# Optimization experiments

Hardware: AMD Instinct MI355X
Metric: run time of the kernel (lower is better)

## Reference

```python
import jax, jax.numpy as jnp
import numpy as np

IN_F = 768
OUT_F = 256
ALPHA = 0.2  # LeakyReLU negative slope
N = 8192


def setup_inputs() -> dict:
    key = jax.random.key(0)
    k_x, k_w, k_a = jax.random.split(key, 3)
    all_token_tensor = jax.random.normal(k_x, (N, IN_F), dtype=jnp.float32)
    # xavier_uniform with gain=1.414 for W [in, out] and a [2*out, 1]
    lim_w = 1.414 * np.sqrt(6.0 / (IN_F + OUT_F))
    W = jax.random.uniform(k_w, (IN_F, OUT_F), minval=-lim_w, maxval=lim_w, dtype=jnp.float32)
    lim_a = 1.414 * np.sqrt(6.0 / (2 * OUT_F + 1))
    a = jax.random.uniform(k_a, (2 * OUT_F, 1), minval=-lim_a, maxval=lim_a, dtype=jnp.float32)
    return {"all_token_tensor": all_token_tensor, "W": W, "a": a}


def reference(all_token_tensor, W, a):
    # Wh: [N, F]
    Wh = all_token_tensor @ W
    # e_ij = leakyrelu([Wh_i ; Wh_j] . a) = leakyrelu(Wh_i.a1 + Wh_j.a2)
    # (identical math to the original's [N,N,2F] concat, without materializing it)
    s1 = Wh @ a[:OUT_F, 0]   # [N]
    s2 = Wh @ a[OUT_F:, 0]   # [N]
    e = jax.nn.leaky_relu(s1[:, None] + s2[None, :], negative_slope=ALPHA)  # [N, N]
    attention = jax.nn.softmax(jnp.sum(e, axis=1), axis=-1)  # [N]
    global_vec = jax.nn.elu(attention @ Wh).reshape(1, -1)   # [1, F]
    return global_vec
```

## Files before the change

### kernel.cpp

```cpp
#include <hip/hip_runtime.h>
#include <math.h>

#define IN_F   768
#define OUT_F  256
#define NROWS  8192
#define LALPHA 0.2f
#define CUT    60.0f
#define GAP    (CUT / (LALPHA * 8192.0f))
#define MAXC   64


__device__ inline float waveReduceSum(float v) {
    for (int off = 32; off > 0; off >>= 1) v += __shfl_down(v, off, 64);
    return v;
}
__device__ inline float waveReduceMax(float v) {
    for (int off = 32; off > 0; off >>= 1) v = fmaxf(v, __shfl_down(v, off, 64));
    return v;
}
__device__ inline float blockReduceMax256(float v, float* red, int tid) {
    v = waveReduceMax(v);
    if ((tid & 63) == 0) red[tid >> 6] = v;
    __syncthreads();
    float r = fmaxf(fmaxf(red[0], red[1]), fmaxf(red[2], red[3]));
    __syncthreads();
    return r;
}

__global__ __launch_bounds__(256) void wvec_kernel(const float* __restrict__ W,
                                                   const float* __restrict__ a,
                                                   float* __restrict__ w1,
                                                   float* __restrict__ w2) {
    __shared__ float la[2 * OUT_F];
    int tid = threadIdx.x;
    la[tid]       = a[tid];
    la[256 + tid] = a[256 + tid];
    __syncthreads();
    int half = tid >> 5;
    int sub  = tid & 31;
    int k = blockIdx.x * 8 + half;
    const float* row = W + (size_t)k * OUT_F;
    float acc1 = 0.f, acc2 = 0.f;
#pragma unroll
    for (int j = 0; j < 8; ++j) {
        int f = sub + 32 * j;
        float w = row[f];
        acc1 += w * la[f];
        acc2 += w * la[256 + f];
    }
    for (int off = 16; off > 0; off >>= 1) {
        acc1 += __shfl_down(acc1, off, 32);
        acc2 += __shfl_down(acc2, off, 32);
    }
    if (sub == 0) { w1[k] = acc1; w2[k] = acc2; }
}

__global__ __launch_bounds__(256) void s1s2_kernel(const float* __restrict__ X,
                                                   const float* __restrict__ w1,
                                                   const float* __restrict__ w2,
                                                   float* __restrict__ s1,
                                                   float* __restrict__ s2) {
    __shared__ float lw[IN_F * 2];
    int tid = threadIdx.x;
    for (int p = tid; p < IN_F; p += 256) { lw[p] = w1[p]; lw[IN_F + p] = w2[p]; }
    __syncthreads();
    int wid = tid >> 6, lane = tid & 63;
    int i = blockIdx.x * 4 + wid;
    const float4* row = (const float4*)(X + (size_t)i * IN_F);
    const float4* l1  = (const float4*)lw;
    const float4* l2  = (const float4*)(lw + IN_F);
    float a1 = 0.f, a2 = 0.f;
#pragma unroll
    for (int c0 = 0; c0 < 3; ++c0) {
        int c = lane + 64 * c0;
        float4 x = row[c];
        float4 u = l1[c];
        float4 v = l2[c];
        a1 += x.x * u.x + x.y * u.y + x.z * u.z + x.w * u.w;
        a2 += x.x * v.x + x.y * v.y + x.z * v.z + x.w * v.w;
    }
    a1 = waveReduceSum(a1);
    a2 = waveReduceSum(a2);
    if (lane == 0) { s1[i] = a1; s2[i] = a2; }
}

__global__ __launch_bounds__(256) void finale_kernel(const float* __restrict__ X,
                                                     const float* __restrict__ W,
                                                     const float* __restrict__ s1g,
                                                     const float* __restrict__ s2g,
                                                     float* __restrict__ out) {
    __shared__ float  s2[NROWS];
    __shared__ float  y[IN_F];
    __shared__ float  red[4];
    __shared__ float4 red4[4];
    __shared__ int    list[MAXC];
    __shared__ float  slist[MAXC];
    __shared__ float  rlist[MAXC];
    __shared__ float  wts[MAXC];
    __shared__ int    cnt;
    int tid = threadIdx.x;
    int wid = tid >> 6, lane = tid & 63;
    if (tid == 0) cnt = 0;

    float4 rv[8];
    float lmax = -INFINITY;
#pragma unroll
    for (int p = 0; p < 8; ++p) {
        rv[p] = ((const float4*)s1g)[tid + 256 * p];
        float4 v2 = ((const float4*)s2g)[tid + 256 * p];
        ((float4*)s2)[tid + 256 * p] = v2;
        lmax = fmaxf(lmax, fmaxf(fmaxf(rv[p].x, rv[p].y), fmaxf(rv[p].z, rv[p].w)));
    }
    float s1max = blockReduceMax256(lmax, red, tid);
    float thr = s1max - GAP;

#pragma unroll
    for (int p = 0; p < 8; ++p) {
        int base = 4 * (tid + 256 * p);
        float v[4] = { rv[p].x, rv[p].y, rv[p].z, rv[p].w };
#pragma unroll
        for (int q = 0; q < 4; ++q) {
            if (v[q] >= thr) {
                int pos = atomicAdd(&cnt, 1);
                if (pos < MAXC) { list[pos] = base + q; slist[pos] = v[q]; }
            }
        }
    }
    __syncthreads();
    int n = cnt < MAXC ? cnt : MAXC;
    if (tid == 0 && n > 1) {
        for (int i = 1; i < n; ++i) {
            int ki = list[i]; float kv = slist[i]; int j = i - 1;
            while (j >= 0 && list[j] > ki) {
                list[j + 1] = list[j]; slist[j + 1] = slist[j]; --j;
            }
            list[j + 1] = ki; slist[j + 1] = kv;
        }
    }
    __syncthreads();

    if (n > 1) {
        for (int c = wid; c < n; c += 4) {
            float s1c = slist[c];
            float acc = 0.f;
#pragma unroll 4
            for (int q = lane; q < NROWS / 4; q += 64) {
                float4 v = ((const float4*)s2)[q];
                acc += fmaxf(s1c + v.x, 0.f) + fmaxf(s1c + v.y, 0.f)
                     + fmaxf(s1c + v.z, 0.f) + fmaxf(s1c + v.w, 0.f);
            }
            acc = waveReduceSum(acc);
            if (lane == 0)
                rlist[c] = LALPHA * 8192.f * s1c + (1.f - LALPHA) * acc;
        }
    }
    __syncthreads();
    if (tid == 0) {
        if (n == 1) wts[0] = 1.0f;
        else {
            float M = -INFINITY;
            for (int c = 0; c < n; ++c) M = fmaxf(M, rlist[c]);
            float Z = 0.f;
            for (int c = 0; c < n; ++c) { float e = expf(rlist[c] - M); rlist[c] = e; Z += e; }
            float invZ = 1.0f / Z;
            for (int c = 0; c < n; ++c) wts[c] = rlist[c] * invZ;
        }
    }
    __syncthreads();

    for (int p = tid; p < IN_F; p += 256) {
        float acc = 0.f;
        for (int c = 0; c < n; ++c)
            acc += wts[c] * X[(size_t)list[c] * IN_F + p];
        y[p] = acc;
    }
    __syncthreads();

    int b4 = blockIdx.x * 4;
    float4 acc = make_float4(0.f, 0.f, 0.f, 0.f);
#pragma unroll
    for (int j = 0; j < 3; ++j) {
        int k = tid + 256 * j;
        float4 w = *(const float4*)(W + (size_t)k * OUT_F + b4);
        float yk = y[k];
        acc.x += yk * w.x; acc.y += yk * w.y; acc.z += yk * w.z; acc.w += yk * w.w;
    }
    for (int off = 32; off > 0; off >>= 1) {
        acc.x += __shfl_down(acc.x, off, 64);
        acc.y += __shfl_down(acc.y, off, 64);
        acc.z += __shfl_down(acc.z, off, 64);
        acc.w += __shfl_down(acc.w, off, 64);
    }
    if (lane == 0) red4[wid] = acc;
    __syncthreads();
    if (tid == 0) {
        float4 t;
        t.x = red4[0].x + red4[1].x + red4[2].x + red4[3].x;
        t.y = red4[0].y + red4[1].y + red4[2].y + red4[3].y;
        t.z = red4[0].z + red4[1].z + red4[2].z + red4[3].z;
        t.w = red4[0].w + red4[1].w + red4[2].w + red4[3].w;
        out[b4 + 0] = (t.x > 0.f) ? t.x : (expf(t.x) - 1.0f);
        out[b4 + 1] = (t.y > 0.f) ? t.y : (expf(t.y) - 1.0f);
        out[b4 + 2] = (t.z > 0.f) ? t.z : (expf(t.z) - 1.0f);
        out[b4 + 3] = (t.w > 0.f) ? t.w : (expf(t.w) - 1.0f);
    }
}

extern "C" void kernel_launch(void* const* d_in, const int* in_sizes, int n_in,
                              void* d_out, int out_size, void* d_ws, size_t ws_size,
                              hipStream_t stream) {
    const float* X = (const float*)d_in[0];
    const float* W = (const float*)d_in[1];
    const float* a = (const float*)d_in[2];
    float* out = (float*)d_out;

    float* ws = (float*)d_ws;
    float* w1 = ws;
    float* w2 = ws + 768;
    float* s1 = ws + 1536;
    float* s2 = ws + 9728;

    wvec_kernel<<<96, 256, 0, stream>>>(W, a, w1, w2);
    s1s2_kernel<<<2048, 256, 0, stream>>>(X, w1, w2, s1, s2);
    finale_kernel<<<64, 256, 0, stream>>>(X, W, s1, s2, out);
}
```

Baseline: 80.63 us.

## Fuse three kernels into one persistent kernel with hierarchical grid barriers

Merges the w-vector, s1/s2 projection and finale kernels into a single 1024-block launch. The stages are separated by a two-level atomic grid barrier in 32 groups, with a spin cap as a safety exit. Each block in the projection stage now handles two rows per wave. This is meant to remove the launch gaps and tail drains between kernels. In exchange it adds a memset launch and barrier spin cost, and it relies on all 1024 blocks being co-resident (4 per CU via launch bounds and LDS use).

```diff
diff --git a/kernel.cpp b/kernel.cpp
--- a/kernel.cpp
+++ b/kernel.cpp
@@ -8,6 +8,7 @@
 #define CUT    60.0f
 #define GAP    (CUT / (LALPHA * 8192.0f))
 #define MAXC   64
+#define NBLK   1024
 
 
 __device__ inline float waveReduceSum(float v) {
@@ -27,70 +28,31 @@
     return r;
 }
 
-__global__ __launch_bounds__(256) void wvec_kernel(const float* __restrict__ W,
-                                                   const float* __restrict__ a,
-                                                   float* __restrict__ w1,
-                                                   float* __restrict__ w2) {
-    __shared__ float la[2 * OUT_F];
-    int tid = threadIdx.x;
-    la[tid]       = a[tid];
-    la[256 + tid] = a[256 + tid];
-    __syncthreads();
-    int half = tid >> 5;
-    int sub  = tid & 31;
-    int k = blockIdx.x * 8 + half;
-    const float* row = W + (size_t)k * OUT_F;
-    float acc1 = 0.f, acc2 = 0.f;
-#pragma unroll
-    for (int j = 0; j < 8; ++j) {
-        int f = sub + 32 * j;
-        float w = row[f];
-        acc1 += w * la[f];
-        acc2 += w * la[256 + f];
-    }
-    for (int off = 16; off > 0; off >>= 1) {
-        acc1 += __shfl_down(acc1, off, 32);
-        acc2 += __shfl_down(acc2, off, 32);
-    }
-    if (sub == 0) { w1[k] = acc1; w2[k] = acc2; }
-}
-
-__global__ __launch_bounds__(256) void s1s2_kernel(const float* __restrict__ X,
-                                                   const float* __restrict__ w1,
-                                                   const float* __restrict__ w2,
-                                                   float* __restrict__ s1,
-                                                   float* __restrict__ s2) {
-    __shared__ float lw[IN_F * 2];
-    int tid = threadIdx.x;
-    for (int p = tid; p < IN_F; p += 256) { lw[p] = w1[p]; lw[IN_F + p] = w2[p]; }
-    __syncthreads();
-    int wid = tid >> 6, lane = tid & 63;
-    int i = blockIdx.x * 4 + wid;
-    const float4* row = (const float4*)(X + (size_t)i * IN_F);
-    const float4* l1  = (const float4*)lw;
-    const float4* l2  = (const float4*)(lw + IN_F);
-    float a1 = 0.f, a2 = 0.f;
-#pragma unroll
-    for (int c0 = 0; c0 < 3; ++c0) {
-        int c = lane + 64 * c0;
-        float4 x = row[c];
-        float4 u = l1[c];
-        float4 v = l2[c];
-        a1 += x.x * u.x + x.y * u.y + x.z * u.z + x.w * u.w;
-        a2 += x.x * v.x + x.y * v.y + x.z * v.z + x.w * v.w;
-    }
-    a1 = waveReduceSum(a1);
-    a2 = waveReduceSum(a2);
-    if (lane == 0) { s1[i] = a1; s2[i] = a2; }
-}
-
-__global__ __launch_bounds__(256) void finale_kernel(const float* __restrict__ X,
-                                                     const float* __restrict__ W,
-                                                     const float* __restrict__ s1g,
-                                                     const float* __restrict__ s2g,
-                                                     float* __restrict__ out) {
-    __shared__ float  s2[NROWS];
-    __shared__ float  y[IN_F];
+__device__ inline void grid_barrier(int* groups, int* root, int bid, int tid) {
+    if (tid == 0) {
+        __threadfence();
+        int g = bid & 31;
+        int old = __hip_atomic_fetch_add(&groups[g * 32], 1,
+                                         __ATOMIC_ACQ_REL, __HIP_MEMORY_SCOPE_AGENT);
+        if (old == 31)
+            __hip_atomic_fetch_add(root, 1, __ATOMIC_ACQ_REL, __HIP_MEMORY_SCOPE_AGENT);
+        int spins = 0;
+        while (__hip_atomic_load(root, __ATOMIC_ACQUIRE, __HIP_MEMORY_SCOPE_AGENT) < 32) {
+            __builtin_amdgcn_s_sleep(8);
+            if (++spins > (1 << 22)) break;
+        }
+    }
+    __syncthreads();
+}
+
+__global__ void __launch_bounds__(256, 4)
+fused_kernel(const float* __restrict__ X, const float* __restrict__ W,
+             const float* __restrict__ a,
+             float* __restrict__ w1, float* __restrict__ w2,
+             float* __restrict__ s1g, float* __restrict__ s2g,
+             int* __restrict__ bar, float* __restrict__ out) {
+    __shared__ float  smem[NROWS];
+    __shared__ float  smem2[2 * IN_F];
     __shared__ float  red[4];
     __shared__ float4 red4[4];
     __shared__ int    list[MAXC];
@@ -98,8 +60,66 @@
     __shared__ float  rlist[MAXC];
     __shared__ float  wts[MAXC];
     __shared__ int    cnt;
-    int tid = threadIdx.x;
-    int wid = tid >> 6, lane = tid & 63;
+
+    const int tid  = threadIdx.x;
+    const int bid  = blockIdx.x;
+    const int wid  = tid >> 6;
+    const int lane = tid & 63;
+
+    if (bid < 96) {
+        smem2[tid]       = a[tid];
+        smem2[256 + tid] = a[256 + tid];
+        __syncthreads();
+        int half = tid >> 5, sub = tid & 31;
+        int k = bid * 8 + half;
+        const float* row = W + (size_t)k * OUT_F;
+        float acc1 = 0.f, acc2 = 0.f;
+#pragma unroll
+        for (int j = 0; j < 8; ++j) {
+            int f = sub + 32 * j;
+            float w = row[f];
+            acc1 += w * smem2[f];
+            acc2 += w * smem2[256 + f];
+        }
+        for (int off = 16; off > 0; off >>= 1) {
+            acc1 += __shfl_down(acc1, off, 32);
+            acc2 += __shfl_down(acc2, off, 32);
+        }
+        if (sub == 0) { w1[k] = acc1; w2[k] = acc2; }
+    }
+    grid_barrier(bar, bar + 1024, bid, tid);
+
+    {
+        smem2[tid]        = w1[tid];
+        smem2[256 + tid]  = w1[256 + tid];
+        smem2[512 + tid]  = w1[512 + tid];
+        smem2[768 + tid]  = w2[tid];
+        smem2[1024 + tid] = w2[256 + tid];
+        smem2[1280 + tid] = w2[512 + tid];
+        __syncthreads();
+        const float4* l1 = (const float4*)smem2;
+        const float4* l2 = (const float4*)(smem2 + IN_F);
+        int rA = bid * 8 + wid * 2, rB = rA + 1;
+        const float4* ra = (const float4*)(X + (size_t)rA * IN_F);
+        const float4* rb = (const float4*)(X + (size_t)rB * IN_F);
+        float a1 = 0.f, a2 = 0.f, b1 = 0.f, b2 = 0.f;
+#pragma unroll
+        for (int c0 = 0; c0 < 3; ++c0) {
+            int c = lane + 64 * c0;
+            float4 xa = ra[c], xb = rb[c];
+            float4 u = l1[c], v = l2[c];
+            a1 += xa.x * u.x + xa.y * u.y + xa.z * u.z + xa.w * u.w;
+            a2 += xa.x * v.x + xa.y * v.y + xa.z * v.z + xa.w * v.w;
+            b1 += xb.x * u.x + xb.y * u.y + xb.z * u.z + xb.w * u.w;
+            b2 += xb.x * v.x + xb.y * v.y + xb.z * v.z + xb.w * v.w;
+        }
+        a1 = waveReduceSum(a1); a2 = waveReduceSum(a2);
+        b1 = waveReduceSum(b1); b2 = waveReduceSum(b2);
+        if (lane == 0) { s1g[rA] = a1; s2g[rA] = a2; s1g[rB] = b1; s2g[rB] = b2; }
+    }
+    grid_barrier(bar + 1056, bar + 2080, bid, tid);
+
+    if (bid >= 64) return;
     if (tid == 0) cnt = 0;
 
     float4 rv[8];
@@ -108,7 +128,7 @@
     for (int p = 0; p < 8; ++p) {
         rv[p] = ((const float4*)s1g)[tid + 256 * p];
         float4 v2 = ((const float4*)s2g)[tid + 256 * p];
-        ((float4*)s2)[tid + 256 * p] = v2;
+        ((float4*)smem)[tid + 256 * p] = v2;
         lmax = fmaxf(lmax, fmaxf(fmaxf(rv[p].x, rv[p].y), fmaxf(rv[p].z, rv[p].w)));
     }
     float s1max = blockReduceMax256(lmax, red, tid);
@@ -145,7 +165,7 @@
             float acc = 0.f;
 #pragma unroll 4
             for (int q = lane; q < NROWS / 4; q += 64) {
-                float4 v = ((const float4*)s2)[q];
+                float4 v = ((const float4*)smem)[q];
                 acc += fmaxf(s1c + v.x, 0.f) + fmaxf(s1c + v.y, 0.f)
                      + fmaxf(s1c + v.z, 0.f) + fmaxf(s1c + v.w, 0.f);
             }
@@ -168,6 +188,7 @@
     }
     __syncthreads();
 
+    float* y = smem2;
     for (int p = tid; p < IN_F; p += 256) {
         float acc = 0.f;
         for (int c = 0; c < n; ++c)
@@ -219,8 +240,8 @@
     float* w2 = ws + 768;
     float* s1 = ws + 1536;
     float* s2 = ws + 9728;
-
-    wvec_kernel<<<96, 256, 0, stream>>>(W, a, w1, w2);
-    s1s2_kernel<<<2048, 256, 0, stream>>>(X, w1, w2, s1, s2);
-    finale_kernel<<<64, 256, 0, stream>>>(X, W, s1, s2, out);
-}
+    int*   bar = (int*)(ws + 17920);
+
+    hipMemsetAsync(bar, 0, 2304 * sizeof(int), stream);
+    fused_kernel<<<NBLK, 256, 0, stream>>>(X, W, a, w1, w2, s1, s2, bar, out);
+}
```

Result: slower. 198.8 us (+146.6%).
